# Kernel tuning notes

Hardware: AMD Instinct MI355X
Metric: run time of the kernel (lower is better)

The kernel has to match this reference:

```python
import jax, jax.numpy as jnp
import numpy as np


def spline_conv(x, src, dst, u, Wk, Wroot, bias, num_nodes):
    # Linear B-spline basis for dim=1, kernel_size=2, degree=1: [(1-u), u]
    # Transform at node level first (cheap GEMM), then gather/blend per edge.
    h0 = x @ Wk[0]           # [N, out]
    h1 = x @ Wk[1]           # [N, out]
    w1 = u[:, 0]             # [E]
    w0 = 1.0 - w1
    msg = w0[:, None] * h0[src] + w1[:, None] * h1[src]   # [E, out]
    agg = jax.ops.segment_sum(msg, dst, num_segments=num_nodes)
    deg = jax.ops.segment_sum(jnp.ones_like(w1), dst, num_segments=num_nodes)
    agg = agg / jnp.maximum(deg, 1.0)[:, None]             # aggr='mean'
    return agg + x @ Wroot + bias


def setup_inputs() -> dict:
    key = jax.random.key(0)
    k = jax.random.split(key, 10)
    N, F_IN, HID, C, E = 100000, 128, 16, 10, 1600000
    x = jax.random.normal(k[0], (N, F_IN), dtype=jnp.float32)
    edge_index = jax.random.randint(k[1], (2, E), 0, N, dtype=jnp.int64)
    edge_attr = jax.random.uniform(k[2], (E, 1), dtype=jnp.float32)
    s1 = 1.0 / np.sqrt(F_IN)
    s2 = 1.0 / np.sqrt(HID)
    W1 = jax.random.uniform(k[3], (2, F_IN, HID), jnp.float32, -s1, s1)
    root1 = jax.random.uniform(k[4], (F_IN, HID), jnp.float32, -s1, s1)
    b1 = jax.random.uniform(k[5], (HID,), jnp.float32, -s1, s1)
    W2 = jax.random.uniform(k[6], (2, HID, C), jnp.float32, -s2, s2)
    root2 = jax.random.uniform(k[7], (HID, C), jnp.float32, -s2, s2)
    b2 = jax.random.uniform(k[8], (C,), jnp.float32, -s2, s2)
    return {"x": x, "edge_index": edge_index, "edge_attr": edge_attr,
            "W1": W1, "root1": root1, "b1": b1,
            "W2": W2, "root2": root2, "b2": b2}


def reference(x, edge_index, edge_attr, W1, root1, b1, W2, root2, b2):
    N = x.shape[0]
    src, dst = edge_index[0], edge_index[1]
    # dropout is identity in eval mode
    h = spline_conv(x, src, dst, edge_attr, W1, root1, b1, N)
    h = jax.nn.elu(h)
    out = spline_conv(h, src, dst, edge_attr, W2, root2, b2, N)
    return out
```

## Files before the change

### kernel.cpp

```cpp
#include <hip/hip_runtime.h>
#include <math.h>


#define SHIFT    7
#define BNODES   128
#define NBUK_MAX 800
#define CAP      2432
#define CHUNK    4096

__device__ __forceinline__ unsigned short f2bf(float f) {
    unsigned int u = __float_as_uint(f);
    u += 0x7FFF + ((u >> 16) & 1);
    return (unsigned short)(u >> 16);
}


__device__ __forceinline__ void gemm_part(
    float* __restrict__ Ws, int gb, int tid,
    const float* __restrict__ x, const float* __restrict__ W1,
    const float* __restrict__ root1, unsigned int* __restrict__ h01i,
    float* __restrict__ xr, int N)
{
    for (int idx = tid; idx < 128 * 48; idx += 256) {
        int k = idx / 48, j = idx % 48;
        int grp = j >> 3, t = j & 7;
        float v;
        switch (grp) {
            case 0: v = W1[k * 16 + t];            break;
            case 1: v = W1[2048 + k * 16 + t];     break;
            case 2: v = root1[k * 16 + t];         break;
            case 3: v = W1[k * 16 + 8 + t];        break;
            case 4: v = W1[2048 + k * 16 + 8 + t]; break;
            default: v = root1[k * 16 + 8 + t];    break;
        }
        Ws[idx] = v;
    }
    __syncthreads();
    int nl   = tid >> 1;
    int half = tid & 1;
    int n = gb * 128 + nl;
    if (n >= N) return;

    float acc[24];
#pragma unroll
    for (int j = 0; j < 24; ++j) acc[j] = 0.f;

    const float4* xrow = (const float4*)(x + (size_t)n * 128);
    const float4* wbase = (const float4*)(Ws + half * 24);
#pragma unroll 8
    for (int k4 = 0; k4 < 32; ++k4) {
        float4 xv = xrow[k4];
        float xs[4] = {xv.x, xv.y, xv.z, xv.w};
#pragma unroll
        for (int kk = 0; kk < 4; ++kk) {
            float xk = xs[kk];
            const float4* w4 = wbase + ((k4 * 4 + kk) * 48) / 4;
#pragma unroll
            for (int q = 0; q < 6; ++q) {
                float4 wv = w4[q];
                acc[q * 4 + 0] += xk * wv.x;
                acc[q * 4 + 1] += xk * wv.y;
                acc[q * 4 + 2] += xk * wv.z;
                acc[q * 4 + 3] += xk * wv.w;
            }
        }
    }
    int cb = half * 8;
#pragma unroll
    for (int t = 0; t < 8; ++t)
        h01i[(size_t)n * 16 + cb + t] =
            (unsigned int)f2bf(acc[t]) | ((unsigned int)f2bf(acc[8 + t]) << 16);
#pragma unroll
    for (int t = 0; t < 8; ++t)
        xr[(size_t)n * 16 + cb + t] = acc[16 + t];
}

__device__ __forceinline__ void bin_part(
    int* __restrict__ smem, int bb, int tid,
    const int* __restrict__ ei, const float* __restrict__ ea,
    int* __restrict__ gcur, unsigned int* __restrict__ staging, int E, int nbuk)
{
    int* bcnt  = smem;
    int* gbase = bcnt + NBUK_MAX;
    for (int i = tid; i < nbuk; i += 256) bcnt[i] = 0;
    __syncthreads();

    int base = bb * CHUNK;
    int lrank[16];
#pragma unroll
    for (int i = 0; i < 16; ++i) {
        int e = base + i * 256 + tid;
        lrank[i] = 0;
        if (e < E) lrank[i] = atomicAdd(&bcnt[ei[E + e] >> SHIFT], 1);
    }
    __syncthreads();
    for (int b = tid; b < nbuk; b += 256) {
        int c = bcnt[b];
        gbase[b] = c ? atomicAdd(&gcur[b], c) : 0;
    }
    __syncthreads();
#pragma unroll
    for (int i = 0; i < 16; ++i) {
        int e = base + i * 256 + tid;
        if (e < E) {
            int s = ei[e];
            int d = ei[E + e];
            int b = d >> SHIFT;
            int p = gbase[b] + lrank[i];
            int wq = (int)(ea[e] * 256.0f + 0.5f);
            if (wq > 255) wq = 255;
            if (p < CAP)
                staging[(size_t)b * CAP + p] =
                    (unsigned int)s | ((unsigned int)wq << 17)
                                    | ((unsigned int)(d & (BNODES - 1)) << 25);
        }
    }
}

__global__ __launch_bounds__(256, 4) void phase1_kernel(
    const float* __restrict__ x, const float* __restrict__ W1,
    const float* __restrict__ root1, unsigned int* __restrict__ h01i,
    float* __restrict__ xr,
    const int* __restrict__ ei, const float* __restrict__ ea,
    int* __restrict__ gcur, unsigned int* __restrict__ staging,
    int N, int E, int nbuk, int binBlocks)
{
    __shared__ float smem[128 * 48];
    int tid = threadIdx.x;
    int bid = blockIdx.x;
    if (bid < binBlocks)
        bin_part((int*)smem, bid, tid, ei, ea, gcur, staging, E, nbuk);
    else
        gemm_part(smem, bid - binBlocks, tid, x, W1, root1, h01i, xr, N);
}

__global__ __launch_bounds__(256) void csr_g1_kernel(
    unsigned int* __restrict__ staging, const int* __restrict__ gcur,
    int* __restrict__ roff, int* __restrict__ cnt,
    const unsigned int* __restrict__ h01i, const float* __restrict__ xr,
    const float* __restrict__ b1, const float* __restrict__ root2,
    const float* __restrict__ b2, unsigned short* __restrict__ hb,
    float* __restrict__ hrb, int N)
{
    __shared__ unsigned int rin[CAP];
    __shared__ unsigned int rout[CAP];
    __shared__ int hist[BNODES];
    __shared__ int sscan[BNODES];
    __shared__ int wcur[BNODES];
    __shared__ float r2s[160];
    __shared__ float b1s[16];
    __shared__ float b2s[10];
    int tid = threadIdx.x;
    int b = blockIdx.x;
    int m = gcur[b];
    if (m > CAP) m = CAP;
    unsigned int* sp = staging + (size_t)b * CAP;

    if (tid < 160) r2s[tid] = root2[tid];
    if (tid < 16)  b1s[tid] = b1[tid];
    if (tid < 10)  b2s[tid] = b2[tid];
    if (tid < BNODES) { hist[tid] = 0; wcur[tid] = 0; }
    __syncthreads();
    for (int k = tid; k < m; k += 256) {
        unsigned int r = sp[k];
        rin[k] = r;
        atomicAdd(&hist[r >> 25], 1);
    }
    __syncthreads();
    if (tid < BNODES) sscan[tid] = hist[tid];
    __syncthreads();
    for (int off = 1; off < BNODES; off <<= 1) {
        int t = (tid < BNODES && tid >= off) ? sscan[tid - off] : 0;
        __syncthreads();
        if (tid < BNODES) sscan[tid] += t;
        __syncthreads();
    }
    for (int k = tid; k < m; k += 256) {
        unsigned int r = rin[k];
        int dl = r >> 25;
        int pos = (sscan[dl] - hist[dl]) + atomicAdd(&wcur[dl], 1);
        rout[pos] = (r & 0x1FFFF) | (((r >> 17) & 0xFF) << 24);
    }
    __syncthreads();
    for (int k = tid; k < m; k += 256) sp[k] = rout[k];
    if (tid < BNODES) {
        int n = b * BNODES + tid;
        if (n < N) {
            roff[n] = b * CAP + (sscan[tid] - hist[tid]);
            cnt[n]  = hist[tid];
        }
    }
    int group = tid >> 4;
    int c     = tid & 15;
#pragma unroll 1
    for (int nn = 0; nn < 8; ++nn) {
        int nl = nn * 16 + group;
        int n = b * BNODES + nl;
        if (n >= N) continue;
        int start = sscan[nl] - hist[nl];
        int mm = hist[nl];
        float acc = 0.f;
#pragma unroll 4
        for (int k = 0; k < mm; ++k) {
            unsigned int rec = rout[start + k];
            float w = (float)(rec >> 17) * (1.0f / 32768.0f);
            unsigned int v = h01i[(size_t)(rec & 0x1FFFF) * 16 + c];
            float a  = __uint_as_float(v << 16);
            float bb = __uint_as_float(v & 0xFFFF0000u);
            acc += a + w * (bb - a);
        }
        float invd = 1.0f / fmaxf((float)mm, 1.0f);
        float hv = acc * invd + xr[(size_t)n * 16 + c] + b1s[c];
        hv = hv > 0.f ? hv : expm1f(hv);
        hb[(size_t)n * 16 + c] = f2bf(hv);

        float r[10];
#pragma unroll
        for (int j = 0; j < 10; ++j) r[j] = hv * r2s[c * 10 + j];
#pragma unroll
        for (int off = 1; off < 16; off <<= 1) {
#pragma unroll
            for (int j = 0; j < 10; ++j) r[j] += __shfl_xor(r[j], off);
        }
        if (c == 0) {
            float* hp = hrb + (size_t)n * 10;
#pragma unroll
            for (int j = 0; j < 10; ++j) hp[j] = r[j] + b2s[j];
        }
    }
}

__global__ __launch_bounds__(256) void gather2f_kernel(
    const unsigned int* __restrict__ staging, const int* __restrict__ roff,
    const int* __restrict__ cnt, const unsigned short* __restrict__ hb,
    const float* __restrict__ hrb, const float* __restrict__ W2,
    float* __restrict__ out, int N)
{
    __shared__ float w2s[320];
    int tid = threadIdx.x;
    for (int idx = tid; idx < 320; idx += 256) w2s[idx] = W2[idx];
    __syncthreads();
    int t = blockIdx.x * 256 + tid;
    int n = t >> 4;
    int c = t & 15;
    if (n >= N) return;
    int start = roff[n];
    int m = cnt[n];
    float p = 0.f, q = 0.f;
#pragma unroll 4
    for (int k = 0; k < m; ++k) {
        unsigned int rec = staging[(size_t)start + k];
        float w = (float)(rec >> 17) * (1.0f / 32768.0f);
        float v = __uint_as_float(((unsigned int)hb[(size_t)(rec & 0x1FFFF) * 16 + c]) << 16);
        p += (1.f - w) * v;
        q += w * v;
    }
    float invd = 1.0f / fmaxf((float)m, 1.0f);
    float o[10];
#pragma unroll
    for (int j = 0; j < 10; ++j)
        o[j] = p * w2s[c * 10 + j] + q * w2s[160 + c * 10 + j];
#pragma unroll
    for (int off = 1; off < 16; off <<= 1) {
#pragma unroll
        for (int j = 0; j < 10; ++j) o[j] += __shfl_xor(o[j], off);
    }
    if (c == 0) {
        float* op = out + (size_t)n * 10;
        const float* hp = hrb + (size_t)n * 10;
#pragma unroll
        for (int j = 0; j < 10; ++j) op[j] = o[j] * invd + hp[j];
    }
}

extern "C" void kernel_launch(void* const* d_in, const int* in_sizes, int n_in,
                              void* d_out, int out_size, void* d_ws, size_t ws_size,
                              hipStream_t stream)
{
    const float* x     = (const float*)d_in[0];
    const int*   ei    = (const int*)d_in[1];
    const float* ea    = (const float*)d_in[2];
    const float* W1    = (const float*)d_in[3];
    const float* root1 = (const float*)d_in[4];
    const float* b1    = (const float*)d_in[5];
    const float* W2    = (const float*)d_in[6];
    const float* root2 = (const float*)d_in[7];
    const float* b2    = (const float*)d_in[8];
    float* out = (float*)d_out;

    int N = in_sizes[0] / 128;
    int E = in_sizes[2];
    int nbuk = (N + BNODES - 1) / BNODES;

    char* ws = (char*)d_ws;
    unsigned int* staging = (unsigned int*)ws;
    unsigned int* h01i = (unsigned int*)(ws + (size_t)nbuk * CAP * 4);
    float* xr    = (float*)(h01i + (size_t)N * 16);
    float* hrb   = xr + (size_t)N * 16;
    unsigned short* hb = (unsigned short*)(hrb + (size_t)N * 10);
    int*   cnt   = (int*)(hb + (size_t)N * 16);
    int*   roff  = cnt + N;
    int*   gcur  = roff + N;

    int nb_e16 = (N * 16 + 255) / 256;
    int gemmBlocks = (N + 127) / 128;
    int binBlocks  = (E + CHUNK - 1) / CHUNK;

    hipMemsetAsync(gcur, 0, (size_t)nbuk * sizeof(int), stream);

    phase1_kernel <<<binBlocks + gemmBlocks, 256, 0, stream>>>(
        x, W1, root1, h01i, xr, ei, ea, gcur, staging, N, E, nbuk, binBlocks);
    csr_g1_kernel <<<nbuk, 256, 0, stream>>>(staging, gcur, roff, cnt, h01i,
                                             xr, b1, root2, b2, hb, hrb, N);
    gather2f_kernel<<<nb_e16, 256, 0, stream>>>(staging, roff, cnt, hb, hrb,
                                                W2, out, N);
}
```

Baseline: 124.3 us.

## Fuse layer-1 gather and layer-2 gather into one cooperative kernel with grid sync

Merges the CSR-build/layer-1 kernel and the layer-2 gather kernel into a single cooperative launch separated by a grid-wide sync. The sorted edge records and the per-node root2 projection stay in LDS, so the staging write-back, roff/cnt arrays and the hrb global buffer are no longer needed. The phase1 kernel's minimum-occupancy hint is also raised from 4 to 6. The risk is that the cooperative launch needs all ~782 blocks resident at once with large LDS use per block; if they cannot all fit, the launch fails. Layer 2 also now runs with one block per 128 nodes, which may give less parallelism than before.

```diff
diff --git a/kernel.cpp b/kernel.cpp
--- a/kernel.cpp
+++ b/kernel.cpp
@@ -1,5 +1,8 @@
 #include <hip/hip_runtime.h>
+#include <hip/hip_cooperative_groups.h>
 #include <math.h>
+
+namespace cg = cooperative_groups;
 
 
 #define SHIFT    7
@@ -117,7 +120,7 @@
     }
 }
 
-__global__ __launch_bounds__(256, 4) void phase1_kernel(
+__global__ __launch_bounds__(256, 6) void phase1_kernel(
     const float* __restrict__ x, const float* __restrict__ W1,
     const float* __restrict__ root1, unsigned int* __restrict__ h01i,
     float* __restrict__ xr,
@@ -134,29 +137,32 @@
         gemm_part(smem, bid - binBlocks, tid, x, W1, root1, h01i, xr, N);
 }
 
-__global__ __launch_bounds__(256) void csr_g1_kernel(
-    unsigned int* __restrict__ staging, const int* __restrict__ gcur,
-    int* __restrict__ roff, int* __restrict__ cnt,
+__global__ __launch_bounds__(256) void csr_g12_kernel(
+    const unsigned int* __restrict__ staging, const int* __restrict__ gcur,
     const unsigned int* __restrict__ h01i, const float* __restrict__ xr,
     const float* __restrict__ b1, const float* __restrict__ root2,
-    const float* __restrict__ b2, unsigned short* __restrict__ hb,
-    float* __restrict__ hrb, int N)
-{
+    const float* __restrict__ b2, const float* __restrict__ W2,
+    unsigned short* __restrict__ hb, float* __restrict__ out, int N)
+{
+    cg::grid_group grid = cg::this_grid();
     __shared__ unsigned int rin[CAP];
     __shared__ unsigned int rout[CAP];
     __shared__ int hist[BNODES];
     __shared__ int sscan[BNODES];
     __shared__ int wcur[BNODES];
     __shared__ float r2s[160];
+    __shared__ float w2s[320];
     __shared__ float b1s[16];
     __shared__ float b2s[10];
+    __shared__ float hrbs[BNODES * 10];
     int tid = threadIdx.x;
     int b = blockIdx.x;
     int m = gcur[b];
     if (m > CAP) m = CAP;
-    unsigned int* sp = staging + (size_t)b * CAP;
+    const unsigned int* sp = staging + (size_t)b * CAP;
 
     if (tid < 160) r2s[tid] = root2[tid];
+    for (int idx = tid; idx < 320; idx += 256) w2s[idx] = W2[idx];
     if (tid < 16)  b1s[tid] = b1[tid];
     if (tid < 10)  b2s[tid] = b2[tid];
     if (tid < BNODES) { hist[tid] = 0; wcur[tid] = 0; }
@@ -182,94 +188,82 @@
         rout[pos] = (r & 0x1FFFF) | (((r >> 17) & 0xFF) << 24);
     }
     __syncthreads();
-    for (int k = tid; k < m; k += 256) sp[k] = rout[k];
-    if (tid < BNODES) {
-        int n = b * BNODES + tid;
-        if (n < N) {
-            roff[n] = b * CAP + (sscan[tid] - hist[tid]);
-            cnt[n]  = hist[tid];
-        }
-    }
+
     int group = tid >> 4;
     int c     = tid & 15;
 #pragma unroll 1
     for (int nn = 0; nn < 8; ++nn) {
         int nl = nn * 16 + group;
         int n = b * BNODES + nl;
-        if (n >= N) continue;
-        int start = sscan[nl] - hist[nl];
-        int mm = hist[nl];
-        float acc = 0.f;
+        if (n < N) {
+            int start = sscan[nl] - hist[nl];
+            int mm = hist[nl];
+            float acc = 0.f;
 #pragma unroll 4
-        for (int k = 0; k < mm; ++k) {
-            unsigned int rec = rout[start + k];
-            float w = (float)(rec >> 17) * (1.0f / 32768.0f);
-            unsigned int v = h01i[(size_t)(rec & 0x1FFFF) * 16 + c];
-            float a  = __uint_as_float(v << 16);
-            float bb = __uint_as_float(v & 0xFFFF0000u);
-            acc += a + w * (bb - a);
-        }
-        float invd = 1.0f / fmaxf((float)mm, 1.0f);
-        float hv = acc * invd + xr[(size_t)n * 16 + c] + b1s[c];
-        hv = hv > 0.f ? hv : expm1f(hv);
-        hb[(size_t)n * 16 + c] = f2bf(hv);
-
-        float r[10];
-#pragma unroll
-        for (int j = 0; j < 10; ++j) r[j] = hv * r2s[c * 10 + j];
-#pragma unroll
-        for (int off = 1; off < 16; off <<= 1) {
-#pragma unroll
-            for (int j = 0; j < 10; ++j) r[j] += __shfl_xor(r[j], off);
-        }
-        if (c == 0) {
-            float* hp = hrb + (size_t)n * 10;
-#pragma unroll
-            for (int j = 0; j < 10; ++j) hp[j] = r[j] + b2s[j];
-        }
-    }
-}
-
-__global__ __launch_bounds__(256) void gather2f_kernel(
-    const unsigned int* __restrict__ staging, const int* __restrict__ roff,
-    const int* __restrict__ cnt, const unsigned short* __restrict__ hb,
-    const float* __restrict__ hrb, const float* __restrict__ W2,
-    float* __restrict__ out, int N)
-{
-    __shared__ float w2s[320];
-    int tid = threadIdx.x;
-    for (int idx = tid; idx < 320; idx += 256) w2s[idx] = W2[idx];
-    __syncthreads();
-    int t = blockIdx.x * 256 + tid;
-    int n = t >> 4;
-    int c = t & 15;
-    if (n >= N) return;
-    int start = roff[n];
-    int m = cnt[n];
-    float p = 0.f, q = 0.f;
+            for (int k = 0; k < mm; ++k) {
+                unsigned int rec = rout[start + k];
+                float w = (float)(rec >> 17) * (1.0f / 32768.0f);
+                unsigned int v = h01i[(size_t)(rec & 0x1FFFF) * 16 + c];
+                float a  = __uint_as_float(v << 16);
+                float bb = __uint_as_float(v & 0xFFFF0000u);
+                acc += a + w * (bb - a);
+            }
+            float invd = 1.0f / fmaxf((float)mm, 1.0f);
+            float hv = acc * invd + xr[(size_t)n * 16 + c] + b1s[c];
+            hv = hv > 0.f ? hv : expm1f(hv);
+            hb[(size_t)n * 16 + c] = f2bf(hv);
+
+            float r[10];
+#pragma unroll
+            for (int j = 0; j < 10; ++j) r[j] = hv * r2s[c * 10 + j];
+#pragma unroll
+            for (int off = 1; off < 16; off <<= 1) {
+#pragma unroll
+                for (int j = 0; j < 10; ++j) r[j] += __shfl_xor(r[j], off);
+            }
+            if (c == 0) {
+#pragma unroll
+                for (int j = 0; j < 10; ++j) hrbs[nl * 10 + j] = r[j] + b2s[j];
+            }
+        }
+    }
+
+    __threadfence();
+    grid.sync();
+
+#pragma unroll 1
+    for (int nn = 0; nn < 8; ++nn) {
+        int nl = nn * 16 + group;
+        int n = b * BNODES + nl;
+        if (n < N) {
+            int start = sscan[nl] - hist[nl];
+            int mm = hist[nl];
+            float p = 0.f, q = 0.f;
 #pragma unroll 4
-    for (int k = 0; k < m; ++k) {
-        unsigned int rec = staging[(size_t)start + k];
-        float w = (float)(rec >> 17) * (1.0f / 32768.0f);
-        float v = __uint_as_float(((unsigned int)hb[(size_t)(rec & 0x1FFFF) * 16 + c]) << 16);
-        p += (1.f - w) * v;
-        q += w * v;
-    }
-    float invd = 1.0f / fmaxf((float)m, 1.0f);
-    float o[10];
-#pragma unroll
-    for (int j = 0; j < 10; ++j)
-        o[j] = p * w2s[c * 10 + j] + q * w2s[160 + c * 10 + j];
-#pragma unroll
-    for (int off = 1; off < 16; off <<= 1) {
-#pragma unroll
-        for (int j = 0; j < 10; ++j) o[j] += __shfl_xor(o[j], off);
-    }
-    if (c == 0) {
-        float* op = out + (size_t)n * 10;
-        const float* hp = hrb + (size_t)n * 10;
-#pragma unroll
-        for (int j = 0; j < 10; ++j) op[j] = o[j] * invd + hp[j];
+            for (int k = 0; k < mm; ++k) {
+                unsigned int rec = rout[start + k];
+                float w = (float)(rec >> 17) * (1.0f / 32768.0f);
+                float v = __uint_as_float(
+                    ((unsigned int)hb[(size_t)(rec & 0x1FFFF) * 16 + c]) << 16);
+                p += (1.f - w) * v;
+                q += w * v;
+            }
+            float invd = 1.0f / fmaxf((float)mm, 1.0f);
+            float o[10];
+#pragma unroll
+            for (int j = 0; j < 10; ++j)
+                o[j] = p * w2s[c * 10 + j] + q * w2s[160 + c * 10 + j];
+#pragma unroll
+            for (int off = 1; off < 16; off <<= 1) {
+#pragma unroll
+                for (int j = 0; j < 10; ++j) o[j] += __shfl_xor(o[j], off);
+            }
+            if (c == 0) {
+                float* op = out + (size_t)n * 10;
+#pragma unroll
+                for (int j = 0; j < 10; ++j) op[j] = o[j] * invd + hrbs[nl * 10 + j];
+            }
+        }
     }
 }
 
@@ -296,13 +290,9 @@
     unsigned int* staging = (unsigned int*)ws;
     unsigned int* h01i = (unsigned int*)(ws + (size_t)nbuk * CAP * 4);
     float* xr    = (float*)(h01i + (size_t)N * 16);
-    float* hrb   = xr + (size_t)N * 16;
-    unsigned short* hb = (unsigned short*)(hrb + (size_t)N * 10);
-    int*   cnt   = (int*)(hb + (size_t)N * 16);
-    int*   roff  = cnt + N;
-    int*   gcur  = roff + N;
-
-    int nb_e16 = (N * 16 + 255) / 256;
+    unsigned short* hb = (unsigned short*)(xr + (size_t)N * 16);
+    int*   gcur  = (int*)(hb + (size_t)N * 16);
+
     int gemmBlocks = (N + 127) / 128;
     int binBlocks  = (E + CHUNK - 1) / CHUNK;
 
@@ -310,8 +300,12 @@
 
     phase1_kernel <<<binBlocks + gemmBlocks, 256, 0, stream>>>(
         x, W1, root1, h01i, xr, ei, ea, gcur, staging, N, E, nbuk, binBlocks);
-    csr_g1_kernel <<<nbuk, 256, 0, stream>>>(staging, gcur, roff, cnt, h01i,
-                                             xr, b1, root2, b2, hb, hrb, N);
-    gather2f_kernel<<<nb_e16, 256, 0, stream>>>(staging, roff, cnt, hb, hrb,
-                                                W2, out, N);
-}
+
+    void* args[] = {
+        (void*)&staging, (void*)&gcur, (void*)&h01i, (void*)&xr,
+        (void*)&b1, (void*)&root2, (void*)&b2, (void*)&W2,
+        (void*)&hb, (void*)&out, (void*)&N
+    };
+    hipLaunchCooperativeKernel((void*)csr_g12_kernel, dim3(nbuk), dim3(256),
+                               args, 0, stream);
+}
```

Result: slower. 280.9 us (+126.0%).
